# Performance work log

Measured on AMD Instinct MI355X. Metric: run time of the kernel, lower is better.

Reference implementation:

```python
import jax, jax.numpy as jnp
import numpy as np

WIN = (9, 9, 9)
EPS = 1e-05


def setup_inputs() -> dict:
    key = jax.random.key(0)
    k1, k2 = jax.random.split(key)
    shape = (2, 1, 160, 160, 160)  # [B, C=1, D, H, W]
    x = jax.random.normal(k1, shape, dtype=jnp.float32)
    y = jax.random.normal(k2, shape, dtype=jnp.float32)
    return {"x": x, "y": y}


def _convn(z, kernel):
    # dense 3D box-sum conv, VALID (inputs are pre-padded), NCDHW layout
    return jax.lax.conv_general_dilated(
        z, kernel, window_strides=(1, 1, 1), padding='VALID',
        dimension_numbers=('NCDHW', 'OIDHW', 'NCDHW'))


def reference(x, y):
    p = tuple(w // 2 for w in WIN)  # (4, 4, 4)
    pad_cfg = ((0, 0), (0, 0), (p[0], p[0]), (p[1], p[1]), (p[2], p[2]))
    kernel = jnp.ones((1, 1) + WIN, dtype=x.dtype)

    x_pad = jnp.pad(x, pad_cfg, mode='edge')      # replicate padding
    y_pad = jnp.pad(y, pad_cfg, mode='edge')
    ones_pad = jnp.pad(jnp.ones_like(x), pad_cfg, mode='edge')

    N = _convn(ones_pad, kernel)                  # local window counts (all = 729 here)
    xm = _convn(x_pad, kernel) / N                # local mean of x
    ym = _convn(y_pad, kernel) / N                # local mean of y
    x2 = _convn(x_pad * x_pad, kernel) / N        # local E[x^2]
    y2 = _convn(y_pad * y_pad, kernel) / N        # local E[y^2]
    xy = _convn(x_pad * y_pad, kernel) / N        # local E[xy]

    cross = xy - xm * ym
    var_x = x2 - xm * xm
    var_y = y2 - ym * ym
    ncc = cross * cross / (var_x * var_y + EPS)
    return -jnp.mean(ncc)
```

## Files before the change

### kernel.cpp

```cpp
#include <hip/hip_runtime.h>

#define DIM 160
#define SLICE (DIM * DIM)
#define TH 16
#define TW 16
#define CD 20

__global__ __launch_bounds__(192, 5)
void lncc_kernel(const float* __restrict__ x, const float* __restrict__ y,
                 float* __restrict__ out)
{
    __shared__ __align__(16) float S[5][24][28];
    __shared__ __align__(16) float T[5][16][28];

    const int t  = threadIdx.x;
    const int w0 = blockIdx.x * TW;
    const int h0 = blockIdx.y * TH;
    const int bz = blockIdx.z;
    const int b   = bz >> 3;
    const int zo0 = (bz & 7) * CD;

    const float* xb = x + (size_t)b * (DIM * SLICE);
    const float* yb = y + (size_t)b * (DIM * SLICE);

    const int h1  = t / 6;
    const int w41 = t - h1 * 6;
    const int gh  = min(max(h0 - 4 + h1, 0), DIM - 1);
    const int gwb = w0 - 4 + 4 * w41;
    const bool fast = (gwb >= 0) && (gwb + 3 < DIM);
    const int jc0 = min(max(gwb + 0, 0), DIM - 1);
    const int jc1 = min(max(gwb + 1, 0), DIM - 1);
    const int jc2 = min(max(gwb + 2, 0), DIM - 1);
    const int jc3 = min(max(gwb + 3, 0), DIM - 1);

    auto load4 = [&](const float* sl) -> float4 {
        const float* row = sl + (size_t)gh * DIM;
        if (fast) return *reinterpret_cast<const float4*>(row + gwb);
        float4 r;
        r.x = row[jc0]; r.y = row[jc1]; r.z = row[jc2]; r.w = row[jc3];
        return r;
    };

    float4 rs0 = {0,0,0,0}, rs1 = {0,0,0,0}, rs2 = {0,0,0,0},
           rs3 = {0,0,0,0}, rs4 = {0,0,0,0};

    if (t < 144) {
        #pragma unroll
        for (int k = -4; k <= 4; ++k) {
            const int z = min(max(zo0 + k, 0), DIM - 1);
            const float* xs = xb + (size_t)z * SLICE;
            const float* ys = yb + (size_t)z * SLICE;
            const float4 xv = load4(xs);
            const float4 yv = load4(ys);
            rs0 += xv; rs1 += yv;
            rs2 += xv * xv; rs3 += yv * yv; rs4 += xv * yv;
        }
    }

    const int c2  = t / 24;
    const int r2  = t - c2 * 24;
    const int w42 = r2 >> 2;
    const int i02 = (r2 & 3) * 4;

    const int i3 = t >> 2;
    const int j3 = (t & 3) * 4;

    float acc = 0.f;

    for (int zo = zo0; zo < zo0 + CD; ++zo) {
        if (t < 144) {
            *reinterpret_cast<float4*>(&S[0][h1][4 * w41]) = rs0;
            *reinterpret_cast<float4*>(&S[1][h1][4 * w41]) = rs1;
            *reinterpret_cast<float4*>(&S[2][h1][4 * w41]) = rs2;
            *reinterpret_cast<float4*>(&S[3][h1][4 * w41]) = rs3;
            *reinterpret_cast<float4*>(&S[4][h1][4 * w41]) = rs4;
        }
        __syncthreads();

        if (t < 120) {
            float4 s = {0,0,0,0};
            #pragma unroll
            for (int k = 0; k < 9; ++k)
                s += *reinterpret_cast<const float4*>(&S[c2][i02 + k][4 * w42]);
            *reinterpret_cast<float4*>(&T[c2][i02][4 * w42]) = s;
            #pragma unroll
            for (int m = 1; m < 4; ++m) {
                s += *reinterpret_cast<const float4*>(&S[c2][i02 + 8 + m][4 * w42])
                   - *reinterpret_cast<const float4*>(&S[c2][i02 + m - 1][4 * w42]);
                *reinterpret_cast<float4*>(&T[c2][i02 + m][4 * w42]) = s;
            }
        }

        if (t < 144 && zo + 1 < zo0 + CD) {
            const int za = min(zo + 5, DIM - 1);
            const int zs = max(zo - 4, 0);
            const float* xsa = xb + (size_t)za * SLICE;
            const float* ysa = yb + (size_t)za * SLICE;
            const float* xss = xb + (size_t)zs * SLICE;
            const float* yss = yb + (size_t)zs * SLICE;
            const float4 xa = load4(xsa), ya = load4(ysa);
            const float4 xs_ = load4(xss), ys_ = load4(yss);
            rs0 += xa - xs_;
            rs1 += ya - ys_;
            rs2 += xa * xa - xs_ * xs_;
            rs3 += ya * ya - ys_ * ys_;
            rs4 += xa * ya - xs_ * ys_;
        }
        __syncthreads();

        if (t < 64) {
            float su[5][4];
            #pragma unroll
            for (int c = 0; c < 5; ++c) {
                const float4 t0 = *reinterpret_cast<const float4*>(&T[c][i3][j3]);
                const float4 t1 = *reinterpret_cast<const float4*>(&T[c][i3][j3 + 4]);
                const float4 t2 = *reinterpret_cast<const float4*>(&T[c][i3][j3 + 8]);
                float s = t0.x + t0.y + t0.z + t0.w + t1.x + t1.y + t1.z + t1.w + t2.x;
                su[c][0] = s;
                s += t2.y - t0.x; su[c][1] = s;
                s += t2.z - t0.y; su[c][2] = s;
                s += t2.w - t0.z; su[c][3] = s;
            }
            const float inv = 1.0f / 729.0f;
            #pragma unroll
            for (int m = 0; m < 4; ++m) {
                const float xm = su[0][m] * inv, ym = su[1][m] * inv;
                const float x2 = su[2][m] * inv, y2 = su[3][m] * inv;
                const float xy = su[4][m] * inv;
                const float cross = xy - xm * ym;
                const float vx = x2 - xm * xm;
                const float vy = y2 - ym * ym;
                acc += cross * cross / (vx * vy + 1e-5f);
            }
        }
    }

    #pragma unroll
    for (int off = 32; off > 0; off >>= 1)
        acc += __shfl_down(acc, off, 64);
    if (t == 0)
        atomicAdd(out, -acc * (1.0f / 8192000.0f));
}

extern "C" void kernel_launch(void* const* d_in, const int* in_sizes, int n_in,
                              void* d_out, int out_size, void* d_ws, size_t ws_size,
                              hipStream_t stream)
{
    const float* x = (const float*)d_in[0];
    const float* y = (const float*)d_in[1];
    float* out = (float*)d_out;

    hipMemsetAsync(out, 0, sizeof(float), stream);

    dim3 grid(DIM / TW, DIM / TH, 2 * (DIM / CD));
    lncc_kernel<<<grid, 192, 0, stream>>>(x, y, out);
}
```

Before: 201.1 us.

## Move depth box-sum to per-thread register ring buffer after 2D in-plane sums

Restructures the separable box filter so each input slice is loaded once (instead of twice, add and subtract) and reduced first in H and W through shared memory. The depth-direction sum is then kept per output voxel in a 9-deep register history ring, with 256 threads each owning one output voxel. The z-chunk doubles to 40 to reduce halo reload overhead, and the block now uses three barriers per slice plus a cross-wave reduction before the atomic. The trade-off is more syncs per slice, more registers for the history, fewer blocks in the grid, and 2D sums computed for 48 slices per 40 outputs.

```diff
diff --git a/kernel.cpp b/kernel.cpp
--- a/kernel.cpp
+++ b/kernel.cpp
@@ -4,21 +4,27 @@
 #define SLICE (DIM * DIM)
 #define TH 16
 #define TW 16
-#define CD 20
+#define CD 40
 
-__global__ __launch_bounds__(192, 5)
+#define SIDX(c,i,j) ((c)*680 + (i)*28 + (j))
+#define TIDX(c,i,j) ((c)*456 + (i)*28 + (j))
+#define UIDX(c,i,j) ((c)*260 + (i)*16 + (j))
+
+__global__ __launch_bounds__(256, 4)
 void lncc_kernel(const float* __restrict__ x, const float* __restrict__ y,
                  float* __restrict__ out)
 {
-    __shared__ __align__(16) float S[5][24][28];
-    __shared__ __align__(16) float T[5][16][28];
+    __shared__ __align__(16) float S[5 * 680];
+    __shared__ __align__(16) float T[5 * 456];
+    __shared__ __align__(16) float U[5 * 260];
+    __shared__ float wsum[4];
 
     const int t  = threadIdx.x;
     const int w0 = blockIdx.x * TW;
     const int h0 = blockIdx.y * TH;
     const int bz = blockIdx.z;
-    const int b   = bz >> 3;
-    const int zo0 = (bz & 7) * CD;
+    const int b   = bz >> 2;
+    const int zo0 = (bz & 3) * CD;
 
     const float* xb = x + (size_t)b * (DIM * SLICE);
     const float* yb = y + (size_t)b * (DIM * SLICE);
@@ -41,22 +47,6 @@
         return r;
     };
 
-    float4 rs0 = {0,0,0,0}, rs1 = {0,0,0,0}, rs2 = {0,0,0,0},
-           rs3 = {0,0,0,0}, rs4 = {0,0,0,0};
-
-    if (t < 144) {
-        #pragma unroll
-        for (int k = -4; k <= 4; ++k) {
-            const int z = min(max(zo0 + k, 0), DIM - 1);
-            const float* xs = xb + (size_t)z * SLICE;
-            const float* ys = yb + (size_t)z * SLICE;
-            const float4 xv = load4(xs);
-            const float4 yv = load4(ys);
-            rs0 += xv; rs1 += yv;
-            rs2 += xv * xv; rs3 += yv * yv; rs4 += xv * yv;
-        }
-    }
-
     const int c2  = t / 24;
     const int r2  = t - c2 * 24;
     const int w42 = r2 >> 2;
@@ -65,72 +55,99 @@
     const int i3 = t >> 2;
     const int j3 = (t & 3) * 4;
 
+    const int i4 = t >> 4;
+    const int j4 = t & 15;
+
+    float hist[9][5];
+    float rs[5] = {0.f, 0.f, 0.f, 0.f, 0.f};
     float acc = 0.f;
 
-    for (int zo = zo0; zo < zo0 + CD; ++zo) {
+    float4 xv = {0,0,0,0}, yv = {0,0,0,0};
+    {
+        const int z0 = min(max(zo0 - 4, 0), DIM - 1);
         if (t < 144) {
-            *reinterpret_cast<float4*>(&S[0][h1][4 * w41]) = rs0;
-            *reinterpret_cast<float4*>(&S[1][h1][4 * w41]) = rs1;
-            *reinterpret_cast<float4*>(&S[2][h1][4 * w41]) = rs2;
-            *reinterpret_cast<float4*>(&S[3][h1][4 * w41]) = rs3;
-            *reinterpret_cast<float4*>(&S[4][h1][4 * w41]) = rs4;
+            xv = load4(xb + (size_t)z0 * SLICE);
+            yv = load4(yb + (size_t)z0 * SLICE);
         }
-        __syncthreads();
+    }
 
-        if (t < 120) {
-            float4 s = {0,0,0,0};
-            #pragma unroll
-            for (int k = 0; k < 9; ++k)
-                s += *reinterpret_cast<const float4*>(&S[c2][i02 + k][4 * w42]);
-            *reinterpret_cast<float4*>(&T[c2][i02][4 * w42]) = s;
-            #pragma unroll
-            for (int m = 1; m < 4; ++m) {
-                s += *reinterpret_cast<const float4*>(&S[c2][i02 + 8 + m][4 * w42])
-                   - *reinterpret_cast<const float4*>(&S[c2][i02 + m - 1][4 * w42]);
-                *reinterpret_cast<float4*>(&T[c2][i02 + m][4 * w42]) = s;
-            }
-        }
+    const int zlast = zo0 + CD + 3;
+    for (int base = zo0 - 4; base <= zlast; base += 9) {
+        #pragma unroll
+        for (int p = 0; p < 9; ++p) {
+            const int zi = base + p;
+            if (zi <= zlast) {
+                if (t < 144) {
+                    const int jw = 4 * w41;
+                    *reinterpret_cast<float4*>(&S[SIDX(0, h1, jw)]) = xv;
+                    *reinterpret_cast<float4*>(&S[SIDX(1, h1, jw)]) = yv;
+                    *reinterpret_cast<float4*>(&S[SIDX(2, h1, jw)]) = xv * xv;
+                    *reinterpret_cast<float4*>(&S[SIDX(3, h1, jw)]) = yv * yv;
+                    *reinterpret_cast<float4*>(&S[SIDX(4, h1, jw)]) = xv * yv;
+                }
+                __syncthreads();
 
-        if (t < 144 && zo + 1 < zo0 + CD) {
-            const int za = min(zo + 5, DIM - 1);
-            const int zs = max(zo - 4, 0);
-            const float* xsa = xb + (size_t)za * SLICE;
-            const float* ysa = yb + (size_t)za * SLICE;
-            const float* xss = xb + (size_t)zs * SLICE;
-            const float* yss = yb + (size_t)zs * SLICE;
-            const float4 xa = load4(xsa), ya = load4(ysa);
-            const float4 xs_ = load4(xss), ys_ = load4(yss);
-            rs0 += xa - xs_;
-            rs1 += ya - ys_;
-            rs2 += xa * xa - xs_ * xs_;
-            rs3 += ya * ya - ys_ * ys_;
-            rs4 += xa * ya - xs_ * ys_;
-        }
-        __syncthreads();
+                if (t < 144 && zi < zlast) {
+                    const int zn = min(max(zi + 1, 0), DIM - 1);
+                    xv = load4(xb + (size_t)zn * SLICE);
+                    yv = load4(yb + (size_t)zn * SLICE);
+                }
 
-        if (t < 64) {
-            float su[5][4];
-            #pragma unroll
-            for (int c = 0; c < 5; ++c) {
-                const float4 t0 = *reinterpret_cast<const float4*>(&T[c][i3][j3]);
-                const float4 t1 = *reinterpret_cast<const float4*>(&T[c][i3][j3 + 4]);
-                const float4 t2 = *reinterpret_cast<const float4*>(&T[c][i3][j3 + 8]);
-                float s = t0.x + t0.y + t0.z + t0.w + t1.x + t1.y + t1.z + t1.w + t2.x;
-                su[c][0] = s;
-                s += t2.y - t0.x; su[c][1] = s;
-                s += t2.z - t0.y; su[c][2] = s;
-                s += t2.w - t0.z; su[c][3] = s;
-            }
-            const float inv = 1.0f / 729.0f;
-            #pragma unroll
-            for (int m = 0; m < 4; ++m) {
-                const float xm = su[0][m] * inv, ym = su[1][m] * inv;
-                const float x2 = su[2][m] * inv, y2 = su[3][m] * inv;
-                const float xy = su[4][m] * inv;
-                const float cross = xy - xm * ym;
-                const float vx = x2 - xm * xm;
-                const float vy = y2 - ym * ym;
-                acc += cross * cross / (vx * vy + 1e-5f);
+                if (t < 120) {
+                    const int jw = 4 * w42;
+                    float4 s = {0,0,0,0};
+                    #pragma unroll
+                    for (int k = 0; k < 9; ++k)
+                        s += *reinterpret_cast<const float4*>(&S[SIDX(c2, i02 + k, jw)]);
+                    *reinterpret_cast<float4*>(&T[TIDX(c2, i02, jw)]) = s;
+                    #pragma unroll
+                    for (int m = 1; m < 4; ++m) {
+                        s += *reinterpret_cast<const float4*>(&S[SIDX(c2, i02 + 8 + m, jw)])
+                           - *reinterpret_cast<const float4*>(&S[SIDX(c2, i02 + m - 1, jw)]);
+                        *reinterpret_cast<float4*>(&T[TIDX(c2, i02 + m, jw)]) = s;
+                    }
+                }
+                __syncthreads();
+
+                if (t < 64) {
+                    #pragma unroll
+                    for (int c = 0; c < 5; ++c) {
+                        const float4 t0 = *reinterpret_cast<const float4*>(&T[TIDX(c, i3, j3)]);
+                        const float4 t1 = *reinterpret_cast<const float4*>(&T[TIDX(c, i3, j3 + 4)]);
+                        const float4 t2 = *reinterpret_cast<const float4*>(&T[TIDX(c, i3, j3 + 8)]);
+                        float4 uo;
+                        float s = t0.x + t0.y + t0.z + t0.w
+                                + t1.x + t1.y + t1.z + t1.w + t2.x;
+                        uo.x = s;
+                        s += t2.y - t0.x; uo.y = s;
+                        s += t2.z - t0.y; uo.z = s;
+                        s += t2.w - t0.z; uo.w = s;
+                        *reinterpret_cast<float4*>(&U[UIDX(c, i3, j3)]) = uo;
+                    }
+                }
+                __syncthreads();
+
+                float u[5];
+                #pragma unroll
+                for (int c = 0; c < 5; ++c) {
+                    u[c] = U[UIDX(c, i4, j4)];
+                    rs[c] += u[c];
+                    hist[p][c] = u[c];
+                }
+                if (zi >= zo0 + 4) {
+                    const float inv = 1.0f / 729.0f;
+                    const float xm = rs[0] * inv, ym = rs[1] * inv;
+                    const float x2 = rs[2] * inv, y2 = rs[3] * inv;
+                    const float xy = rs[4] * inv;
+                    const float cross = xy - xm * ym;
+                    const float vx = x2 - xm * xm;
+                    const float vy = y2 - ym * ym;
+                    acc += cross * cross / (vx * vy + 1e-5f);
+                    const int po = (p + 1) % 9;
+                    #pragma unroll
+                    for (int c = 0; c < 5; ++c)
+                        rs[c] -= hist[po][c];
+                }
             }
         }
     }
@@ -138,8 +155,13 @@
     #pragma unroll
     for (int off = 32; off > 0; off >>= 1)
         acc += __shfl_down(acc, off, 64);
-    if (t == 0)
-        atomicAdd(out, -acc * (1.0f / 8192000.0f));
+    const int wave = t >> 6;
+    if ((t & 63) == 0) wsum[wave] = acc;
+    __syncthreads();
+    if (t == 0) {
+        const float s = wsum[0] + wsum[1] + wsum[2] + wsum[3];
+        atomicAdd(out, -s * (1.0f / 8192000.0f));
+    }
 }
 
 extern "C" void kernel_launch(void* const* d_in, const int* in_sizes, int n_in,
@@ -153,5 +175,5 @@
     hipMemsetAsync(out, 0, sizeof(float), stream);
 
     dim3 grid(DIM / TW, DIM / TH, 2 * (DIM / CD));
-    lncc_kernel<<<grid, 192, 0, stream>>>(x, y, out);
+    lncc_kernel<<<grid, 256, 0, stream>>>(x, y, out);
 }
```

Result: faster. 163.5 us (-18.7%).
